# Kernel optimization log

Measured on AMD Instinct MI355X. Metric: run time of the kernel, lower is better.

## Reference

```python
import jax, jax.numpy as jnp
import numpy as np

B, S, H, D, DM = 2, 512, 8, 32, 256  # batch, seq_len, n_head, d_k, d_model


def setup_inputs() -> dict:
    key = jax.random.key(0)
    ks = jax.random.split(key, 8)
    scale = 0.02
    return {
        "hidden_states": jax.random.normal(ks[0], (B, S, DM), dtype=jnp.float32),
        "rpe": jax.random.normal(ks[1], (B, S, S, D), dtype=jnp.float32),
        "w_q": jax.random.normal(ks[2], (DM, H * D), dtype=jnp.float32) * scale,
        "w_k": jax.random.normal(ks[3], (DM, H * D), dtype=jnp.float32) * scale,
        "w_v": jax.random.normal(ks[4], (DM, H * D), dtype=jnp.float32) * scale,
        "fc_w": jax.random.normal(ks[5], (H * D, DM), dtype=jnp.float32) * scale,
        "fc_b": jnp.zeros((DM,), dtype=jnp.float32),
        "ln_w": jnp.ones((DM,), dtype=jnp.float32),
        "ln_b": jnp.zeros((DM,), dtype=jnp.float32),
        "station_num": 256,
    }


def reference(hidden_states, rpe, w_q, w_k, w_v, fc_w, fc_b, ln_w, ln_b, station_num):
    b, s, dm = hidden_states.shape
    d = rpe.shape[-1]
    h = w_q.shape[1] // d

    def heads(x, w):
        # (b, s, dm) @ (dm, h*d) -> (b, h, s, d)
        return (x @ w).reshape(b, s, h, d).transpose(0, 2, 1, 3)

    q = heads(hidden_states, w_q)
    k = heads(hidden_states, w_k)
    v = heads(hidden_states, w_v)

    # torch: (q.unsqueeze(2) * k.unsqueeze(3) * rpe.unsqueeze(1)).sum(-1)
    # scores[b,h,i,j] = sum_d q[b,h,j,d] * k[b,h,i,d] * rpe[b,i,j,d]
    scores = jnp.einsum('bhjd,bhid,bijd->bhij', q, k, rpe) / jnp.sqrt(jnp.float32(d))

    # shielded mask: column j visible if j < station_num, plus the diagonal
    col = jnp.arange(s) < station_num                  # (s,)
    mask = col[None, :] | jnp.eye(s, dtype=bool)        # (s, s)
    scores = jnp.where(mask[None, None], scores, jnp.float32(-1e10))

    attn = jax.nn.softmax(scores, axis=-1)              # (b, h, s, s)
    out = jnp.einsum('bhij,bhjd->bhid', attn, v)        # (b, h, s, d)
    out = out.transpose(0, 2, 1, 3).reshape(b, s, h * d)

    ctx = out @ fc_w + fc_b + hidden_states             # residual
    mu = jnp.mean(ctx, axis=-1, keepdims=True)
    var = jnp.mean(jnp.square(ctx - mu), axis=-1, keepdims=True)
    ctx = (ctx - mu) / jnp.sqrt(var + 1e-6) * ln_w + ln_b
    return ctx
```

## Files before the change

### kernel.cpp

```cpp
#include <hip/hip_runtime.h>
#include <hip/hip_bf16.h>

#define B_  2
#define S_  512
#define H_  8
#define D_  32
#define DM_ 256
#define HD_ 256
#define NROW 4
#define TI  2
#define HC  2
#define NR  (TI * HC)

__global__ __launch_bounds__(256) void qkv_kernel(
    const float* __restrict__ hid, const float* __restrict__ wq,
    const float* __restrict__ wk, const float* __restrict__ wv,
    float* __restrict__ qo, float* __restrict__ ko, float* __restrict__ vo)
{
  __shared__ float hs[NROW][DM_];
  const int r0 = blockIdx.x * NROW;
  const float* w   = (blockIdx.y == 0) ? wq : (blockIdx.y == 1) ? wk : wv;
  float*       out = (blockIdx.y == 0) ? qo : (blockIdx.y == 1) ? ko : vo;
  const float mulf = (blockIdx.y == 0) ? 0.17677669529663687f : 1.0f;
  const int tid = threadIdx.x;

  for (int idx = tid; idx < NROW * DM_; idx += 256)
    hs[idx >> 8][idx & 255] = hid[r0 * DM_ + idx];
  __syncthreads();

  float acc[NROW] = {0.f, 0.f, 0.f, 0.f};
  const float* wp = w + tid;
  #pragma unroll 8
  for (int c4 = 0; c4 < DM_ / 4; ++c4) {
    const float w0 = wp[(4 * c4 + 0) * HD_];
    const float w1 = wp[(4 * c4 + 1) * HD_];
    const float w2 = wp[(4 * c4 + 2) * HD_];
    const float w3 = wp[(4 * c4 + 3) * HD_];
    #pragma unroll
    for (int r = 0; r < NROW; ++r) {
      const float4 hv = reinterpret_cast<const float4*>(&hs[r][0])[c4];
      acc[r] = fmaf(hv.x, w0, acc[r]);
      acc[r] = fmaf(hv.y, w1, acc[r]);
      acc[r] = fmaf(hv.z, w2, acc[r]);
      acc[r] = fmaf(hv.w, w3, acc[r]);
    }
  }
  const int h = tid >> 5, d = tid & 31;
  #pragma unroll
  for (int r = 0; r < NROW; ++r) {
    const int g = r0 + r;
    const int b = g >> 9, s = g & (S_ - 1);
    out[((b * H_ + h) * S_ + s) * D_ + d] = acc[r] * mulf;
  }
}

__device__ __forceinline__ float red4(float x) {
  int i;
  i = __builtin_amdgcn_mov_dpp(__float_as_int(x), 0xB1, 0xf, 0xf, true);
  x += __int_as_float(i);
  i = __builtin_amdgcn_mov_dpp(__float_as_int(x), 0x4E, 0xf, 0xf, true);
  x += __int_as_float(i);
  return x;
}

__global__ __launch_bounds__(256, 4) void attn_kernel(
    const float* __restrict__ rpe, const float* __restrict__ q_ws,
    const float* __restrict__ k_ws, const float* __restrict__ v_ws,
    const int* __restrict__ station_p, float* __restrict__ o_ws)
{
  __shared__ float p_smem[NR * S_];
  __shared__ float sums[NR];

  const int tid  = threadIdx.x;
  const int w    = tid >> 6, lane = tid & 63;
  const int j4   = lane >> 2, dq = lane & 3;
  const int j8   = lane >> 3, dc = lane & 7;
  const int n    = blockIdx.x;
  const int hg   = (n >> 3) & 3;
  const int t    = (n & 7) | ((n >> 5) << 3);
  const int b    = t >> 8;
  const int i0   = (t & 255) * TI;
  const int h0   = hg * HC;
  const int HS   = S_ * D_;

  int station = station_p[0];
  station = station > S_ ? S_ : (station < 0 ? 0 : station);

  const float* qb = q_ws + (size_t)((b * H_ + h0) * S_) * D_;
  const float* kb = k_ws + (size_t)((b * H_ + h0) * S_ + i0) * D_;
  const float* vb = v_ws + (size_t)((b * H_ + h0) * S_) * D_;
  const float* rb = rpe + ((size_t)b * S_ + i0) * S_ * D_;

  float4 kf[HC][TI][2];
  #pragma unroll
  for (int hh = 0; hh < HC; ++hh)
    #pragma unroll
    for (int ii = 0; ii < TI; ++ii) {
      kf[hh][ii][0] = *reinterpret_cast<const float4*>(kb + hh * HS + ii * D_ + dq * 8);
      kf[hh][ii][1] = *reinterpret_cast<const float4*>(kb + hh * HS + ii * D_ + dq * 8 + 4);
    }

  for (int jb = w * 16; jb < station; jb += 64) {
    const int j  = jb + j4;
    const int jc = j < S_ ? j : S_ - 1;
    float4 q[HC][2];
    #pragma unroll
    for (int hh = 0; hh < HC; ++hh) {
      q[hh][0] = *reinterpret_cast<const float4*>(qb + hh * HS + jc * D_ + dq * 8);
      q[hh][1] = *reinterpret_cast<const float4*>(qb + hh * HS + jc * D_ + dq * 8 + 4);
    }
    float4 rv[TI][2];
    #pragma unroll
    for (int ii = 0; ii < TI; ++ii) {
      rv[ii][0] = *reinterpret_cast<const float4*>(rb + ii * HS + jc * D_ + dq * 8);
      rv[ii][1] = *reinterpret_cast<const float4*>(rb + ii * HS + jc * D_ + dq * 8 + 4);
    }
    #pragma unroll
    for (int hh = 0; hh < HC; ++hh)
      #pragma unroll
      for (int ii = 0; ii < TI; ++ii) {
        float s = q[hh][0].x * kf[hh][ii][0].x * rv[ii][0].x;
        s = fmaf(q[hh][0].y * kf[hh][ii][0].y, rv[ii][0].y, s);
        s = fmaf(q[hh][0].z * kf[hh][ii][0].z, rv[ii][0].z, s);
        s = fmaf(q[hh][0].w * kf[hh][ii][0].w, rv[ii][0].w, s);
        s = fmaf(q[hh][1].x * kf[hh][ii][1].x, rv[ii][1].x, s);
        s = fmaf(q[hh][1].y * kf[hh][ii][1].y, rv[ii][1].y, s);
        s = fmaf(q[hh][1].z * kf[hh][ii][1].z, rv[ii][1].z, s);
        s = fmaf(q[hh][1].w * kf[hh][ii][1].w, rv[ii][1].w, s);
        s = red4(s);
        if (dq == 0 && j < station) p_smem[(hh * TI + ii) * S_ + j] = s;
      }
  }
  if (w == 0 && j4 < TI) {
    const int j = i0 + j4;
    if (j >= station) {
      const float4 r0 = *reinterpret_cast<const float4*>(rb + j4 * HS + j * D_ + dq * 8);
      const float4 r1 = *reinterpret_cast<const float4*>(rb + j4 * HS + j * D_ + dq * 8 + 4);
      #pragma unroll
      for (int hh = 0; hh < HC; ++hh) {
        const float4 q0 = *reinterpret_cast<const float4*>(qb + hh * HS + j * D_ + dq * 8);
        const float4 q1 = *reinterpret_cast<const float4*>(qb + hh * HS + j * D_ + dq * 8 + 4);
        const float4 k0 = *reinterpret_cast<const float4*>(kb + hh * HS + j4 * D_ + dq * 8);
        const float4 k1 = *reinterpret_cast<const float4*>(kb + hh * HS + j4 * D_ + dq * 8 + 4);
        float s = q0.x * k0.x * r0.x;
        s = fmaf(q0.y * k0.y, r0.y, s);
        s = fmaf(q0.z * k0.z, r0.z, s);
        s = fmaf(q0.w * k0.w, r0.w, s);
        s = fmaf(q1.x * k1.x, r1.x, s);
        s = fmaf(q1.y * k1.y, r1.y, s);
        s = fmaf(q1.z * k1.z, r1.z, s);
        s = fmaf(q1.w * k1.w, r1.w, s);
        s = red4(s);
        if (dq == 0) p_smem[(hh * TI + j4) * S_ + j] = s;
      }
    }
  }
  __syncthreads();

  {
    const int r  = w;
    const int ii = r & (TI - 1);
    const int ig = i0 + ii;
    const bool dx = (ig >= station);
    float m = -1e30f;
    for (int jj = lane; jj < station; jj += 64) m = fmaxf(m, p_smem[r * S_ + jj]);
    const float dv = dx ? p_smem[r * S_ + ig] : -1e30f;
    m = fmaxf(m, dv);
    #pragma unroll
    for (int o = 32; o; o >>= 1) m = fmaxf(m, __shfl_xor(m, o, 64));
    float sum = 0.f;
    for (int jj = lane; jj < station; jj += 64) {
      const float e = __expf(p_smem[r * S_ + jj] - m);
      p_smem[r * S_ + jj] = e;
      sum += e;
    }
    #pragma unroll
    for (int o = 32; o; o >>= 1) sum += __shfl_xor(sum, o, 64);
    if (dx) {
      const float e = __expf(dv - m);
      sum += e;
      if (lane == 0) p_smem[r * S_ + ig] = e;
    }
    if (lane == 0) sums[r] = sum;
  }
  __syncthreads();

  float4 acc[HC][TI];
  #pragma unroll
  for (int hh = 0; hh < HC; ++hh)
    #pragma unroll
    for (int ii = 0; ii < TI; ++ii) acc[hh][ii] = make_float4(0.f, 0.f, 0.f, 0.f);

  for (int jb = w * 8; jb < station; jb += 32) {
    const int j  = jb + j8;
    const int jc = j < S_ ? j : S_ - 1;
    float4 v4[HC];
    #pragma unroll
    for (int hh = 0; hh < HC; ++hh)
      v4[hh] = *reinterpret_cast<const float4*>(vb + hh * HS + jc * D_ + dc * 4);
    #pragma unroll
    for (int hh = 0; hh < HC; ++hh)
      #pragma unroll
      for (int ii = 0; ii < TI; ++ii) {
        float pv = 0.f;
        if (j < station) pv = p_smem[(hh * TI + ii) * S_ + j];
        acc[hh][ii].x = fmaf(pv, v4[hh].x, acc[hh][ii].x);
        acc[hh][ii].y = fmaf(pv, v4[hh].y, acc[hh][ii].y);
        acc[hh][ii].z = fmaf(pv, v4[hh].z, acc[hh][ii].z);
        acc[hh][ii].w = fmaf(pv, v4[hh].w, acc[hh][ii].w);
      }
  }
  if (w == 0 && j8 == 0) {
    #pragma unroll
    for (int ii = 0; ii < TI; ++ii) {
      const int ig = i0 + ii;
      if (ig >= station) {
        #pragma unroll
        for (int hh = 0; hh < HC; ++hh) {
          const float pv = p_smem[(hh * TI + ii) * S_ + ig];
          const float4 v4 = *reinterpret_cast<const float4*>(vb + hh * HS + ig * D_ + dc * 4);
          acc[hh][ii].x = fmaf(pv, v4.x, acc[hh][ii].x);
          acc[hh][ii].y = fmaf(pv, v4.y, acc[hh][ii].y);
          acc[hh][ii].z = fmaf(pv, v4.z, acc[hh][ii].z);
          acc[hh][ii].w = fmaf(pv, v4.w, acc[hh][ii].w);
        }
      }
    }
  }
  __syncthreads();

  float4* redv = reinterpret_cast<float4*>(p_smem);
  #pragma unroll
  for (int hh = 0; hh < HC; ++hh)
    #pragma unroll
    for (int ii = 0; ii < TI; ++ii) {
      const int r = hh * TI + ii;
      float4 a = acc[hh][ii];
      a.x += __shfl_xor(a.x, 8);
      a.y += __shfl_xor(a.y, 8);
      a.z += __shfl_xor(a.z, 8);
      a.w += __shfl_xor(a.w, 8);
      if ((j8 & 1) == 0)
        redv[((w * 4 + (j8 >> 1)) * NR + r) * 8 + dc] = a;
    }
  __syncthreads();
  if (tid < NR * 8) {
    const int r = tid >> 3, d4 = tid & 7;
    float4 a = make_float4(0.f, 0.f, 0.f, 0.f);
    #pragma unroll
    for (int g = 0; g < 16; ++g) {
      const float4 x = redv[(g * NR + r) * 8 + d4];
      a.x += x.x; a.y += x.y; a.z += x.z; a.w += x.w;
    }
    const float inv = 1.f / sums[r];
    a.x *= inv; a.y *= inv; a.z *= inv; a.w *= inv;
    const int hh = r >> 1, ii = r & 1;
    reinterpret_cast<float4*>(
        o_ws + (size_t)((b * H_ + h0 + hh) * S_ + i0 + ii) * D_)[d4] = a;
  }
}

__global__ __launch_bounds__(256) void fc_ln_kernel(
    const float* __restrict__ o_ws, const float* __restrict__ fc_w,
    const float* __restrict__ fc_b, const float* __restrict__ hid,
    const float* __restrict__ ln_w, const float* __restrict__ ln_b,
    float* __restrict__ out)
{
  __shared__ float orow[NROW][HD_];
  __shared__ float red[NROW][4];
  const int tid = threadIdx.x;
  const int r0 = blockIdx.x * NROW;

  for (int idx = tid; idx < NROW * HD_; idx += 256) {
    const int r = idx >> 8, m = idx & 255;
    const int g = r0 + r;
    const int b = g >> 9, i = g & (S_ - 1);
    orow[r][m] = o_ws[((b * H_ + (m >> 5)) * S_ + i) * D_ + (m & 31)];
  }
  __syncthreads();

  float acc[NROW] = {0.f, 0.f, 0.f, 0.f};
  const float* wp = fc_w + tid;
  #pragma unroll 8
  for (int n4 = 0; n4 < HD_ / 4; ++n4) {
    const float w0 = wp[(4 * n4 + 0) * DM_];
    const float w1 = wp[(4 * n4 + 1) * DM_];
    const float w2 = wp[(4 * n4 + 2) * DM_];
    const float w3 = wp[(4 * n4 + 3) * DM_];
    #pragma unroll
    for (int r = 0; r < NROW; ++r) {
      const float4 ov = reinterpret_cast<const float4*>(&orow[r][0])[n4];
      acc[r] = fmaf(ov.x, w0, acc[r]);
      acc[r] = fmaf(ov.y, w1, acc[r]);
      acc[r] = fmaf(ov.z, w2, acc[r]);
      acc[r] = fmaf(ov.w, w3, acc[r]);
    }
  }
  const float bias = fc_b[tid];
  #pragma unroll
  for (int r = 0; r < NROW; ++r) acc[r] += bias + hid[(r0 + r) * DM_ + tid];

  const int w = tid >> 6, lane = tid & 63;
  float mu[NROW];
  #pragma unroll
  for (int r = 0; r < NROW; ++r) {
    float s = acc[r];
    #pragma unroll
    for (int o = 32; o; o >>= 1) s += __shfl_xor(s, o, 64);
    if (lane == 0) red[r][w] = s;
  }
  __syncthreads();
  #pragma unroll
  for (int r = 0; r < NROW; ++r)
    mu[r] = (red[r][0] + red[r][1] + red[r][2] + red[r][3]) * (1.f / DM_);
  __syncthreads();
  #pragma unroll
  for (int r = 0; r < NROW; ++r) {
    const float dd = acc[r] - mu[r];
    float s = dd * dd;
    #pragma unroll
    for (int o = 32; o; o >>= 1) s += __shfl_xor(s, o, 64);
    if (lane == 0) red[r][w] = s;
  }
  __syncthreads();
  const float lw = ln_w[tid], lb = ln_b[tid];
  #pragma unroll
  for (int r = 0; r < NROW; ++r) {
    const float var = (red[r][0] + red[r][1] + red[r][2] + red[r][3]) * (1.f / DM_);
    out[(r0 + r) * DM_ + tid] =
        (acc[r] - mu[r]) * rsqrtf(var + 1e-6f) * lw + lb;
  }
}

extern "C" void kernel_launch(void* const* d_in, const int* in_sizes, int n_in,
                              void* d_out, int out_size, void* d_ws, size_t ws_size,
                              hipStream_t stream) {
  const float* hid = (const float*)d_in[0];
  const float* rpe = (const float*)d_in[1];
  const float* wq  = (const float*)d_in[2];
  const float* wk  = (const float*)d_in[3];
  const float* wv  = (const float*)d_in[4];
  const float* fcw = (const float*)d_in[5];
  const float* fcb = (const float*)d_in[6];
  const float* lnw = (const float*)d_in[7];
  const float* lnb = (const float*)d_in[8];
  const int* station = (const int*)d_in[9];
  float* out = (float*)d_out;

  const size_t per = (size_t)B_ * H_ * S_ * D_;
  float* q_ws = (float*)d_ws;
  float* k_ws = q_ws + per;
  float* v_ws = k_ws + per;
  float* o_ws = v_ws + per;

  dim3 gA(B_ * S_ / NROW, 3);
  qkv_kernel<<<gA, 256, 0, stream>>>(hid, wq, wk, wv, q_ws, k_ws, v_ws);
  attn_kernel<<<B_ * (S_ / TI) * (H_ / HC), 256, 0, stream>>>(
      rpe, q_ws, k_ws, v_ws, station, o_ws);
  fc_ln_kernel<<<B_ * S_ / NROW, 256, 0, stream>>>(o_ws, fcw, fcb, hid, lnw, lnb, out);
}
```

Baseline: 156.7 us.

## Fuse attention with FC+LayerNorm, one block per query row over all heads

```diff
diff --git a/kernel.cpp b/kernel.cpp
--- a/kernel.cpp
+++ b/kernel.cpp
@@ -8,16 +8,13 @@
 #define DM_ 256
 #define HD_ 256
 #define NROW 4
-#define TI  2
-#define HC  2
-#define NR  (TI * HC)
 
 __global__ __launch_bounds__(256) void qkv_kernel(
     const float* __restrict__ hid, const float* __restrict__ wq,
     const float* __restrict__ wk, const float* __restrict__ wv,
     float* __restrict__ qo, float* __restrict__ ko, float* __restrict__ vo)
 {
-  __shared__ float hs[NROW][DM_];
+  __shared__ __align__(16) float hs[NROW][DM_];
   const int r0 = blockIdx.x * NROW;
   const float* w   = (blockIdx.y == 0) ? wq : (blockIdx.y == 1) ? wk : wv;
   float*       out = (blockIdx.y == 0) ? qo : (blockIdx.y == 1) ? ko : vo;
@@ -63,108 +60,97 @@
   return x;
 }
 
-__global__ __launch_bounds__(256, 4) void attn_kernel(
+__global__ __launch_bounds__(256, 4) void attn_fused_kernel(
     const float* __restrict__ rpe, const float* __restrict__ q_ws,
     const float* __restrict__ k_ws, const float* __restrict__ v_ws,
-    const int* __restrict__ station_p, float* __restrict__ o_ws)
+    const int* __restrict__ station_p, const float* __restrict__ fc_w,
+    const float* __restrict__ fc_b, const float* __restrict__ hid,
+    const float* __restrict__ ln_w, const float* __restrict__ ln_b,
+    float* __restrict__ out)
 {
-  __shared__ float p_smem[NR * S_];
-  __shared__ float sums[NR];
+  __shared__ __align__(16) float p_smem[H_ * S_];
+  __shared__ __align__(16) float ks[H_ * D_];
+  __shared__ __align__(16) float orow[HD_];
+  __shared__ float sums[H_];
+  __shared__ float redm[4];
+  __shared__ float redvr[4];
 
   const int tid  = threadIdx.x;
   const int w    = tid >> 6, lane = tid & 63;
   const int j4   = lane >> 2, dq = lane & 3;
   const int j8   = lane >> 3, dc = lane & 7;
   const int n    = blockIdx.x;
-  const int hg   = (n >> 3) & 3;
-  const int t    = (n & 7) | ((n >> 5) << 3);
-  const int b    = t >> 8;
-  const int i0   = (t & 255) * TI;
-  const int h0   = hg * HC;
+  const int b    = n >> 9;
+  const int i    = n & (S_ - 1);
   const int HS   = S_ * D_;
 
   int station = station_p[0];
   station = station > S_ ? S_ : (station < 0 ? 0 : station);
 
-  const float* qb = q_ws + (size_t)((b * H_ + h0) * S_) * D_;
-  const float* kb = k_ws + (size_t)((b * H_ + h0) * S_ + i0) * D_;
-  const float* vb = v_ws + (size_t)((b * H_ + h0) * S_) * D_;
-  const float* rb = rpe + ((size_t)b * S_ + i0) * S_ * D_;
-
-  float4 kf[HC][TI][2];
-  #pragma unroll
-  for (int hh = 0; hh < HC; ++hh)
-    #pragma unroll
-    for (int ii = 0; ii < TI; ++ii) {
-      kf[hh][ii][0] = *reinterpret_cast<const float4*>(kb + hh * HS + ii * D_ + dq * 8);
-      kf[hh][ii][1] = *reinterpret_cast<const float4*>(kb + hh * HS + ii * D_ + dq * 8 + 4);
-    }
+  const float* qb = q_ws + (size_t)(b * H_) * S_ * D_;
+  const float* kb = k_ws + (size_t)(b * H_) * S_ * D_;
+  const float* vb = v_ws + (size_t)(b * H_) * S_ * D_;
+  const float* rb = rpe + ((size_t)b * S_ + i) * S_ * D_;
+
+  {
+    const int h = tid >> 5, d = tid & 31;
+    ks[tid] = kb[h * HS + i * D_ + d];
+  }
+  __syncthreads();
 
   for (int jb = w * 16; jb < station; jb += 64) {
     const int j  = jb + j4;
     const int jc = j < S_ ? j : S_ - 1;
-    float4 q[HC][2];
-    #pragma unroll
-    for (int hh = 0; hh < HC; ++hh) {
-      q[hh][0] = *reinterpret_cast<const float4*>(qb + hh * HS + jc * D_ + dq * 8);
-      q[hh][1] = *reinterpret_cast<const float4*>(qb + hh * HS + jc * D_ + dq * 8 + 4);
-    }
-    float4 rv[TI][2];
-    #pragma unroll
-    for (int ii = 0; ii < TI; ++ii) {
-      rv[ii][0] = *reinterpret_cast<const float4*>(rb + ii * HS + jc * D_ + dq * 8);
-      rv[ii][1] = *reinterpret_cast<const float4*>(rb + ii * HS + jc * D_ + dq * 8 + 4);
-    }
-    #pragma unroll
-    for (int hh = 0; hh < HC; ++hh)
-      #pragma unroll
-      for (int ii = 0; ii < TI; ++ii) {
-        float s = q[hh][0].x * kf[hh][ii][0].x * rv[ii][0].x;
-        s = fmaf(q[hh][0].y * kf[hh][ii][0].y, rv[ii][0].y, s);
-        s = fmaf(q[hh][0].z * kf[hh][ii][0].z, rv[ii][0].z, s);
-        s = fmaf(q[hh][0].w * kf[hh][ii][0].w, rv[ii][0].w, s);
-        s = fmaf(q[hh][1].x * kf[hh][ii][1].x, rv[ii][1].x, s);
-        s = fmaf(q[hh][1].y * kf[hh][ii][1].y, rv[ii][1].y, s);
-        s = fmaf(q[hh][1].z * kf[hh][ii][1].z, rv[ii][1].z, s);
-        s = fmaf(q[hh][1].w * kf[hh][ii][1].w, rv[ii][1].w, s);
-        s = red4(s);
-        if (dq == 0 && j < station) p_smem[(hh * TI + ii) * S_ + j] = s;
-      }
-  }
-  if (w == 0 && j4 < TI) {
-    const int j = i0 + j4;
-    if (j >= station) {
-      const float4 r0 = *reinterpret_cast<const float4*>(rb + j4 * HS + j * D_ + dq * 8);
-      const float4 r1 = *reinterpret_cast<const float4*>(rb + j4 * HS + j * D_ + dq * 8 + 4);
-      #pragma unroll
-      for (int hh = 0; hh < HC; ++hh) {
-        const float4 q0 = *reinterpret_cast<const float4*>(qb + hh * HS + j * D_ + dq * 8);
-        const float4 q1 = *reinterpret_cast<const float4*>(qb + hh * HS + j * D_ + dq * 8 + 4);
-        const float4 k0 = *reinterpret_cast<const float4*>(kb + hh * HS + j4 * D_ + dq * 8);
-        const float4 k1 = *reinterpret_cast<const float4*>(kb + hh * HS + j4 * D_ + dq * 8 + 4);
-        float s = q0.x * k0.x * r0.x;
-        s = fmaf(q0.y * k0.y, r0.y, s);
-        s = fmaf(q0.z * k0.z, r0.z, s);
-        s = fmaf(q0.w * k0.w, r0.w, s);
-        s = fmaf(q1.x * k1.x, r1.x, s);
-        s = fmaf(q1.y * k1.y, r1.y, s);
-        s = fmaf(q1.z * k1.z, r1.z, s);
-        s = fmaf(q1.w * k1.w, r1.w, s);
-        s = red4(s);
-        if (dq == 0) p_smem[(hh * TI + j4) * S_ + j] = s;
-      }
-    }
-  }
-  __syncthreads();
-
-  {
-    const int r  = w;
-    const int ii = r & (TI - 1);
-    const int ig = i0 + ii;
-    const bool dx = (ig >= station);
+    const float4 r0 = *reinterpret_cast<const float4*>(rb + jc * D_ + dq * 8);
+    const float4 r1 = *reinterpret_cast<const float4*>(rb + jc * D_ + dq * 8 + 4);
+    #pragma unroll
+    for (int hh = 0; hh < H_; ++hh) {
+      const float4 q0 = *reinterpret_cast<const float4*>(qb + hh * HS + jc * D_ + dq * 8);
+      const float4 q1 = *reinterpret_cast<const float4*>(qb + hh * HS + jc * D_ + dq * 8 + 4);
+      const float4 k0 = *reinterpret_cast<const float4*>(&ks[hh * D_ + dq * 8]);
+      const float4 k1 = *reinterpret_cast<const float4*>(&ks[hh * D_ + dq * 8 + 4]);
+      float s = q0.x * k0.x * r0.x;
+      s = fmaf(q0.y * k0.y, r0.y, s);
+      s = fmaf(q0.z * k0.z, r0.z, s);
+      s = fmaf(q0.w * k0.w, r0.w, s);
+      s = fmaf(q1.x * k1.x, r1.x, s);
+      s = fmaf(q1.y * k1.y, r1.y, s);
+      s = fmaf(q1.z * k1.z, r1.z, s);
+      s = fmaf(q1.w * k1.w, r1.w, s);
+      s = red4(s);
+      if (dq == 0 && j < station) p_smem[hh * S_ + j] = s;
+    }
+  }
+  if (w == 0 && j4 == 0 && i >= station) {
+    const float4 r0 = *reinterpret_cast<const float4*>(rb + i * D_ + dq * 8);
+    const float4 r1 = *reinterpret_cast<const float4*>(rb + i * D_ + dq * 8 + 4);
+    #pragma unroll
+    for (int hh = 0; hh < H_; ++hh) {
+      const float4 q0 = *reinterpret_cast<const float4*>(qb + hh * HS + i * D_ + dq * 8);
+      const float4 q1 = *reinterpret_cast<const float4*>(qb + hh * HS + i * D_ + dq * 8 + 4);
+      const float4 k0 = *reinterpret_cast<const float4*>(&ks[hh * D_ + dq * 8]);
+      const float4 k1 = *reinterpret_cast<const float4*>(&ks[hh * D_ + dq * 8 + 4]);
+      float s = q0.x * k0.x * r0.x;
+      s = fmaf(q0.y * k0.y, r0.y, s);
+      s = fmaf(q0.z * k0.z, r0.z, s);
+      s = fmaf(q0.w * k0.w, r0.w, s);
+      s = fmaf(q1.x * k1.x, r1.x, s);
+      s = fmaf(q1.y * k1.y, r1.y, s);
+      s = fmaf(q1.z * k1.z, r1.z, s);
+      s = fmaf(q1.w * k1.w, r1.w, s);
+      s = red4(s);
+      if (dq == 0) p_smem[hh * S_ + i] = s;
+    }
+  }
+  __syncthreads();
+
+  const bool dx = (i >= station);
+  #pragma unroll
+  for (int rr = 0; rr < 2; ++rr) {
+    const int r = w + rr * 4;
     float m = -1e30f;
     for (int jj = lane; jj < station; jj += 64) m = fmaxf(m, p_smem[r * S_ + jj]);
-    const float dv = dx ? p_smem[r * S_ + ig] : -1e30f;
+    const float dv = dx ? p_smem[r * S_ + i] : -1e30f;
     m = fmaxf(m, dv);
     #pragma unroll
     for (int o = 32; o; o >>= 1) m = fmaxf(m, __shfl_xor(m, o, 64));
@@ -179,157 +165,103 @@
     if (dx) {
       const float e = __expf(dv - m);
       sum += e;
-      if (lane == 0) p_smem[r * S_ + ig] = e;
+      if (lane == 0) p_smem[r * S_ + i] = e;
     }
     if (lane == 0) sums[r] = sum;
   }
   __syncthreads();
 
-  float4 acc[HC][TI];
-  #pragma unroll
-  for (int hh = 0; hh < HC; ++hh)
-    #pragma unroll
-    for (int ii = 0; ii < TI; ++ii) acc[hh][ii] = make_float4(0.f, 0.f, 0.f, 0.f);
+  float4 acc[H_];
+  #pragma unroll
+  for (int hh = 0; hh < H_; ++hh) acc[hh] = make_float4(0.f, 0.f, 0.f, 0.f);
 
   for (int jb = w * 8; jb < station; jb += 32) {
     const int j  = jb + j8;
     const int jc = j < S_ ? j : S_ - 1;
-    float4 v4[HC];
-    #pragma unroll
-    for (int hh = 0; hh < HC; ++hh)
-      v4[hh] = *reinterpret_cast<const float4*>(vb + hh * HS + jc * D_ + dc * 4);
-    #pragma unroll
-    for (int hh = 0; hh < HC; ++hh)
-      #pragma unroll
-      for (int ii = 0; ii < TI; ++ii) {
-        float pv = 0.f;
-        if (j < station) pv = p_smem[(hh * TI + ii) * S_ + j];
-        acc[hh][ii].x = fmaf(pv, v4[hh].x, acc[hh][ii].x);
-        acc[hh][ii].y = fmaf(pv, v4[hh].y, acc[hh][ii].y);
-        acc[hh][ii].z = fmaf(pv, v4[hh].z, acc[hh][ii].z);
-        acc[hh][ii].w = fmaf(pv, v4[hh].w, acc[hh][ii].w);
-      }
-  }
-  if (w == 0 && j8 == 0) {
-    #pragma unroll
-    for (int ii = 0; ii < TI; ++ii) {
-      const int ig = i0 + ii;
-      if (ig >= station) {
-        #pragma unroll
-        for (int hh = 0; hh < HC; ++hh) {
-          const float pv = p_smem[(hh * TI + ii) * S_ + ig];
-          const float4 v4 = *reinterpret_cast<const float4*>(vb + hh * HS + ig * D_ + dc * 4);
-          acc[hh][ii].x = fmaf(pv, v4.x, acc[hh][ii].x);
-          acc[hh][ii].y = fmaf(pv, v4.y, acc[hh][ii].y);
-          acc[hh][ii].z = fmaf(pv, v4.z, acc[hh][ii].z);
-          acc[hh][ii].w = fmaf(pv, v4.w, acc[hh][ii].w);
-        }
-      }
+    #pragma unroll
+    for (int hh = 0; hh < H_; ++hh) {
+      const float4 v4 = *reinterpret_cast<const float4*>(vb + hh * HS + jc * D_ + dc * 4);
+      float pv = 0.f;
+      if (j < station) pv = p_smem[hh * S_ + j];
+      acc[hh].x = fmaf(pv, v4.x, acc[hh].x);
+      acc[hh].y = fmaf(pv, v4.y, acc[hh].y);
+      acc[hh].z = fmaf(pv, v4.z, acc[hh].z);
+      acc[hh].w = fmaf(pv, v4.w, acc[hh].w);
+    }
+  }
+  if (w == 0 && j8 == 0 && dx) {
+    #pragma unroll
+    for (int hh = 0; hh < H_; ++hh) {
+      const float pv = p_smem[hh * S_ + i];
+      const float4 v4 = *reinterpret_cast<const float4*>(vb + hh * HS + i * D_ + dc * 4);
+      acc[hh].x = fmaf(pv, v4.x, acc[hh].x);
+      acc[hh].y = fmaf(pv, v4.y, acc[hh].y);
+      acc[hh].z = fmaf(pv, v4.z, acc[hh].z);
+      acc[hh].w = fmaf(pv, v4.w, acc[hh].w);
     }
   }
   __syncthreads();
 
   float4* redv = reinterpret_cast<float4*>(p_smem);
   #pragma unroll
-  for (int hh = 0; hh < HC; ++hh)
-    #pragma unroll
-    for (int ii = 0; ii < TI; ++ii) {
-      const int r = hh * TI + ii;
-      float4 a = acc[hh][ii];
-      a.x += __shfl_xor(a.x, 8);
-      a.y += __shfl_xor(a.y, 8);
-      a.z += __shfl_xor(a.z, 8);
-      a.w += __shfl_xor(a.w, 8);
-      if ((j8 & 1) == 0)
-        redv[((w * 4 + (j8 >> 1)) * NR + r) * 8 + dc] = a;
-    }
-  __syncthreads();
-  if (tid < NR * 8) {
+  for (int hh = 0; hh < H_; ++hh) {
+    float4 a = acc[hh];
+    #pragma unroll
+    for (int o = 8; o <= 32; o <<= 1) {
+      a.x += __shfl_xor(a.x, o, 64);
+      a.y += __shfl_xor(a.y, o, 64);
+      a.z += __shfl_xor(a.z, o, 64);
+      a.w += __shfl_xor(a.w, o, 64);
+    }
+    if (j8 == 0) redv[(w * H_ + hh) * 8 + dc] = a;
+  }
+  __syncthreads();
+  if (tid < H_ * 8) {
     const int r = tid >> 3, d4 = tid & 7;
     float4 a = make_float4(0.f, 0.f, 0.f, 0.f);
     #pragma unroll
-    for (int g = 0; g < 16; ++g) {
-      const float4 x = redv[(g * NR + r) * 8 + d4];
+    for (int g = 0; g < 4; ++g) {
+      const float4 x = redv[(g * H_ + r) * 8 + d4];
       a.x += x.x; a.y += x.y; a.z += x.z; a.w += x.w;
     }
     const float inv = 1.f / sums[r];
-    a.x *= inv; a.y *= inv; a.z *= inv; a.w *= inv;
-    const int hh = r >> 1, ii = r & 1;
-    reinterpret_cast<float4*>(
-        o_ws + (size_t)((b * H_ + h0 + hh) * S_ + i0 + ii) * D_)[d4] = a;
-  }
-}
-
-__global__ __launch_bounds__(256) void fc_ln_kernel(
-    const float* __restrict__ o_ws, const float* __restrict__ fc_w,
-    const float* __restrict__ fc_b, const float* __restrict__ hid,
-    const float* __restrict__ ln_w, const float* __restrict__ ln_b,
-    float* __restrict__ out)
-{
-  __shared__ float orow[NROW][HD_];
-  __shared__ float red[NROW][4];
-  const int tid = threadIdx.x;
-  const int r0 = blockIdx.x * NROW;
-
-  for (int idx = tid; idx < NROW * HD_; idx += 256) {
-    const int r = idx >> 8, m = idx & 255;
-    const int g = r0 + r;
-    const int b = g >> 9, i = g & (S_ - 1);
-    orow[r][m] = o_ws[((b * H_ + (m >> 5)) * S_ + i) * D_ + (m & 31)];
-  }
-  __syncthreads();
-
-  float acc[NROW] = {0.f, 0.f, 0.f, 0.f};
+    orow[r * D_ + d4 * 4 + 0] = a.x * inv;
+    orow[r * D_ + d4 * 4 + 1] = a.y * inv;
+    orow[r * D_ + d4 * 4 + 2] = a.z * inv;
+    orow[r * D_ + d4 * 4 + 3] = a.w * inv;
+  }
+  __syncthreads();
+
+  float fca = 0.f;
   const float* wp = fc_w + tid;
   #pragma unroll 8
   for (int n4 = 0; n4 < HD_ / 4; ++n4) {
-    const float w0 = wp[(4 * n4 + 0) * DM_];
-    const float w1 = wp[(4 * n4 + 1) * DM_];
-    const float w2 = wp[(4 * n4 + 2) * DM_];
-    const float w3 = wp[(4 * n4 + 3) * DM_];
-    #pragma unroll
-    for (int r = 0; r < NROW; ++r) {
-      const float4 ov = reinterpret_cast<const float4*>(&orow[r][0])[n4];
-      acc[r] = fmaf(ov.x, w0, acc[r]);
-      acc[r] = fmaf(ov.y, w1, acc[r]);
-      acc[r] = fmaf(ov.z, w2, acc[r]);
-      acc[r] = fmaf(ov.w, w3, acc[r]);
-    }
-  }
-  const float bias = fc_b[tid];
-  #pragma unroll
-  for (int r = 0; r < NROW; ++r) acc[r] += bias + hid[(r0 + r) * DM_ + tid];
-
-  const int w = tid >> 6, lane = tid & 63;
-  float mu[NROW];
-  #pragma unroll
-  for (int r = 0; r < NROW; ++r) {
-    float s = acc[r];
+    const float4 ov = reinterpret_cast<const float4*>(orow)[n4];
+    fca = fmaf(ov.x, wp[(4 * n4 + 0) * DM_], fca);
+    fca = fmaf(ov.y, wp[(4 * n4 + 1) * DM_], fca);
+    fca = fmaf(ov.z, wp[(4 * n4 + 2) * DM_], fca);
+    fca = fmaf(ov.w, wp[(4 * n4 + 3) * DM_], fca);
+  }
+  fca += fc_b[tid] + hid[(size_t)n * DM_ + tid];
+
+  {
+    float s = fca;
     #pragma unroll
     for (int o = 32; o; o >>= 1) s += __shfl_xor(s, o, 64);
-    if (lane == 0) red[r][w] = s;
-  }
-  __syncthreads();
-  #pragma unroll
-  for (int r = 0; r < NROW; ++r)
-    mu[r] = (red[r][0] + red[r][1] + red[r][2] + red[r][3]) * (1.f / DM_);
-  __syncthreads();
-  #pragma unroll
-  for (int r = 0; r < NROW; ++r) {
-    const float dd = acc[r] - mu[r];
+    if (lane == 0) redm[w] = s;
+  }
+  __syncthreads();
+  const float mu = (redm[0] + redm[1] + redm[2] + redm[3]) * (1.f / DM_);
+  const float dd = fca - mu;
+  {
     float s = dd * dd;
     #pragma unroll
     for (int o = 32; o; o >>= 1) s += __shfl_xor(s, o, 64);
-    if (lane == 0) red[r][w] = s;
-  }
-  __syncthreads();
-  const float lw = ln_w[tid], lb = ln_b[tid];
-  #pragma unroll
-  for (int r = 0; r < NROW; ++r) {
-    const float var = (red[r][0] + red[r][1] + red[r][2] + red[r][3]) * (1.f / DM_);
-    out[(r0 + r) * DM_ + tid] =
-        (acc[r] - mu[r]) * rsqrtf(var + 1e-6f) * lw + lb;
-  }
+    if (lane == 0) redvr[w] = s;
+  }
+  __syncthreads();
+  const float var = (redvr[0] + redvr[1] + redvr[2] + redvr[3]) * (1.f / DM_);
+  out[(size_t)n * DM_ + tid] = dd * rsqrtf(var + 1e-6f) * ln_w[tid] + ln_b[tid];
 }
 
 extern "C" void kernel_launch(void* const* d_in, const int* in_sizes, int n_in,
@@ -351,11 +283,9 @@
   float* q_ws = (float*)d_ws;
   float* k_ws = q_ws + per;
   float* v_ws = k_ws + per;
-  float* o_ws = v_ws + per;
 
   dim3 gA(B_ * S_ / NROW, 3);
   qkv_kernel<<<gA, 256, 0, stream>>>(hid, wq, wk, wv, q_ws, k_ws, v_ws);
-  attn_kernel<<<B_ * (S_ / TI) * (H_ / HC), 256, 0, stream>>>(
-      rpe, q_ws, k_ws, v_ws, station, o_ws);
-  fc_ln_kernel<<<B_ * S_ / NROW, 256, 0, stream>>>(o_ws, fcw, fcb, hid, lnw, lnb, out);
-}
+  attn_fused_kernel<<<B_ * S_, 256, 0, stream>>>(
+      rpe, q_ws, k_ws, v_ws, station, fcw, fcb, hid, lnw, lnb, out);
+}
```

Result: faster. 151.8 us (-3.1%).
